# Kernel tuning notes

Hardware: AMD Instinct MI355X
Metric: run time of the kernel (lower is better)

Reference implementation:

```python
import jax, jax.numpy as jnp
import numpy as np

N_NODES = 100000
N_EDGES = 1600000
N_GRAPH = 100
IN_DIM = 64
LATENT = 128
STEPS = 2
MLP_LAYERS = 2
OUT_GLOBALS = 1
EPS = 1e-5  # haiku LayerNorm default


def setup_inputs() -> dict:
    key = jax.random.key(0)
    ks = jax.random.split(key, 8)
    nodes = jax.random.normal(ks[0], (N_NODES, IN_DIM), jnp.float32)
    senders = jax.random.randint(ks[1], (N_EDGES,), 0, N_NODES, jnp.int32)
    receivers = jax.random.randint(ks[2], (N_EDGES,), 0, N_NODES, jnp.int32)
    # 100 graphs of 1000 nodes each: jnp.repeat(arange(n_graph), n_node)
    graph_ids = (jnp.arange(N_NODES) // (N_NODES // N_GRAPH)).astype(jnp.int32)
    embed_w = jax.random.normal(ks[3], (IN_DIM, LATENT), jnp.float32) / np.sqrt(IN_DIM).astype(np.float32)
    embed_b = jnp.zeros((LATENT,), jnp.float32)
    mlp_w = jax.random.normal(ks[4], (STEPS, MLP_LAYERS, LATENT, LATENT), jnp.float32) / np.sqrt(LATENT).astype(np.float32)
    mlp_b = jnp.zeros((STEPS, MLP_LAYERS, LATENT), jnp.float32)
    ln_scale = jnp.ones((STEPS, LATENT), jnp.float32)
    ln_offset = jnp.zeros((STEPS, LATENT), jnp.float32)
    dec_w = jax.random.normal(ks[5], (LATENT, OUT_GLOBALS), jnp.float32) / np.sqrt(LATENT).astype(np.float32)
    dec_b = jnp.zeros((OUT_GLOBALS,), jnp.float32)
    return dict(nodes=nodes, senders=senders, receivers=receivers, graph_ids=graph_ids,
                embed_w=embed_w, embed_b=embed_b, mlp_w=mlp_w, mlp_b=mlp_b,
                ln_scale=ln_scale, ln_offset=ln_offset, dec_w=dec_w, dec_b=dec_b)


def _layernorm(x, scale, offset):
    mu = jnp.mean(x, axis=-1, keepdims=True)
    var = jnp.var(x, axis=-1, keepdims=True)
    return (x - mu) * jax.lax.rsqrt(var + EPS) * scale + offset


def reference(nodes, senders, receivers, graph_ids, embed_w, embed_b,
              mlp_w, mlp_b, ln_scale, ln_offset, dec_w, dec_b):
    n = nodes.shape[0]
    # jraph.GraphConvolution(add_self_edges=True, symmetric_normalization=True)
    self_loop = jnp.arange(n, dtype=senders.dtype)
    conv_s = jnp.concatenate([senders, self_loop])
    conv_r = jnp.concatenate([receivers, self_loop])
    ones_e = jnp.ones(conv_s.shape[0], jnp.float32)
    inv_sqrt_sdeg = jax.lax.rsqrt(jnp.maximum(jax.ops.segment_sum(ones_e, conv_s, n), 1.0))
    inv_sqrt_rdeg = jax.lax.rsqrt(jnp.maximum(jax.ops.segment_sum(ones_e, conv_r, n), 1.0))

    # embedder: hk.Linear on nodes
    h = nodes @ embed_w + embed_b

    for s in range(STEPS):
        # update_node_fn: MLP (dropout_rate=0 -> identity dropout)
        x = h
        for l in range(MLP_LAYERS):
            x = jax.nn.relu(x @ mlp_w[s, l] + mlp_b[s, l])
        # symmetric-normalized segment_sum aggregation with self-edges
        x = x * inv_sqrt_sdeg[:, None]
        x = jax.ops.segment_sum(x[conv_s], conv_r, num_segments=n)  # [n, LATENT]
        x = x * inv_sqrt_rdeg[:, None]
        h = x + h  # skip connection (add_graphs_tuples)
        h = _layernorm(h, ln_scale[s], ln_offset[s])

    # segment_mean pooling over graphs
    counts = jnp.maximum(jax.ops.segment_sum(jnp.ones(n, jnp.float32), graph_ids, N_GRAPH), 1.0)
    pooled = jax.ops.segment_sum(h, graph_ids, num_segments=N_GRAPH) / counts[:, None]
    # decoder: hk.Linear on pooled globals
    return pooled @ dec_w + dec_b  # [N_GRAPH, OUT_GLOBALS]
```

## Files before the change

kernel.cpp:

```cpp
#include <hip/hip_runtime.h>
#include <hip/hip_bf16.h>


#define N_NODES 100000
#define N_EDGES 1600000
#define N_GRAPH 100
#define NPG     1000
#define LATENT  128

#define NPART   4
#define PSIZE   (N_NODES / NPART)
#define NSLICE  64
#define ESLICE  (N_EDGES / NSLICE)

#define SCAN_CHUNK 2048
#define SCAN_NB    ((N_NODES + SCAN_CHUNK - 1) / SCAN_CHUNK)

typedef __attribute__((ext_vector_type(8))) short short8;
typedef __attribute__((ext_vector_type(4))) float f32x4;

__device__ __forceinline__ unsigned short f2bf(float f) {
    union { float f; unsigned int u; } v; v.f = f;
    unsigned int r = v.u + 0x7fff + ((v.u >> 16) & 1);
    return (unsigned short)(r >> 16);
}
__device__ __forceinline__ float bf2f(unsigned short u) {
    union { unsigned int u; float f; } v; v.u = ((unsigned int)u) << 16;
    return v.f;
}

__global__ __launch_bounds__(1024) void k_hist2(const int* __restrict__ senders,
                                                const int* __restrict__ receivers,
                                                unsigned short* __restrict__ ps16,
                                                unsigned short* __restrict__ pr16) {
    __shared__ unsigned int cs[PSIZE / 2];
    __shared__ unsigned int cr[PSIZE / 2];
    int rg = blockIdx.x & (NPART - 1), sl = blockIdx.x >> 2;
    int lo = rg * PSIZE;
    for (int i = threadIdx.x; i < PSIZE / 2; i += 1024) { cs[i] = 0; cr[i] = 0; }
    __syncthreads();
    int e0 = sl * ESLICE;
    for (int e = e0 + threadIdx.x; e < e0 + ESLICE; e += 1024) {
        int s = senders[e] - lo;
        if ((unsigned)s < PSIZE) atomicAdd(&cs[s >> 1], 1u << ((s & 1) * 16));
        int r = receivers[e] - lo;
        if ((unsigned)r < PSIZE) atomicAdd(&cr[r >> 1], 1u << ((r & 1) * 16));
    }
    __syncthreads();
    size_t base = (size_t)(rg * NSLICE + sl) * PSIZE;
    for (int i = threadIdx.x; i < PSIZE; i += 1024) {
        ps16[base + i] = (unsigned short)((cs[i >> 1] >> ((i & 1) * 16)) & 0xffff);
        pr16[base + i] = (unsigned short)((cr[i >> 1] >> ((i & 1) * 16)) & 0xffff);
    }
}

__global__ __launch_bounds__(256) void k_scan_slices(const unsigned short* __restrict__ ps16,
                                                     unsigned short* __restrict__ pr16,
                                                     int* __restrict__ deg_r,
                                                     float* __restrict__ inv_s,
                                                     float* __restrict__ inv_r) {
    int n = blockIdx.x * 256 + threadIdx.x;
    if (n >= N_NODES) return;
    int rg = n / PSIZE, i = n - rg * PSIZE;
    size_t base = (size_t)rg * NSLICE * PSIZE + i;
    int run = 0, ss = 0;
#pragma unroll 4
    for (int sl = 0; sl < NSLICE; sl++) {
        size_t idx = base + (size_t)sl * PSIZE;
        int v = pr16[idx];
        pr16[idx] = (unsigned short)run;
        run += v;
        ss += ps16[idx];
    }
    deg_r[n] = run;
    inv_r[n] = rsqrtf((float)(run + 1));
    inv_s[n] = rsqrtf((float)(ss + 1));
}

__global__ __launch_bounds__(256) void k_scan_block(const int* __restrict__ deg,
                                                    int* __restrict__ blocksums, int n) {
    int b = blockIdx.x, t = threadIdx.x;
    int base = b * SCAN_CHUNK + t * 8;
    int s = 0;
#pragma unroll
    for (int j = 0; j < 8; j++) { int i = base + j; if (i < n) s += deg[i]; }
    __shared__ int wsum[4];
#pragma unroll
    for (int off = 32; off > 0; off >>= 1) s += __shfl_down(s, off, 64);
    if ((t & 63) == 0) wsum[t >> 6] = s;
    __syncthreads();
    if (t == 0) blocksums[b] = wsum[0] + wsum[1] + wsum[2] + wsum[3];
}

__global__ __launch_bounds__(256) void k_scan_apply(const int* __restrict__ deg,
                                                    const int* __restrict__ blocksums,
                                                    int* __restrict__ row_start, int n) {
    __shared__ int boff_s;
    int b = blockIdx.x, t = threadIdx.x;
    if (t < 64) {
        int v = (t < b && t < SCAN_NB) ? blocksums[t] : 0;
#pragma unroll
        for (int off = 32; off > 0; off >>= 1) v += __shfl_down(v, off, 64);
        if (t == 0) boff_s = v;
    }
    int base = b * SCAN_CHUNK + t * 8;
    int v[8]; int tsum = 0;
#pragma unroll
    for (int j = 0; j < 8; j++) { int i = base + j; v[j] = (i < n) ? deg[i] : 0; tsum += v[j]; }
    __shared__ int wtot[4];
    int inc = tsum;
#pragma unroll
    for (int off = 1; off < 64; off <<= 1) {
        int u = __shfl_up(inc, off, 64);
        if ((t & 63) >= off) inc += u;
    }
    if ((t & 63) == 63) wtot[t >> 6] = inc;
    __syncthreads();
    int wbase = 0;
    for (int w = 0; w < (t >> 6); w++) wbase += wtot[w];
    int running = boff_s + wbase + (inc - tsum);
#pragma unroll
    for (int j = 0; j < 8; j++) {
        int i = base + j;
        if (i < n) {
            row_start[i] = running;
            running += v[j];
            if (i == n - 1) row_start[n] = running;
        }
    }
}

__global__ __launch_bounds__(1024) void k_fill2(const int* __restrict__ senders,
                                                const int* __restrict__ receivers,
                                                const unsigned short* __restrict__ pr16,
                                                const int* __restrict__ row_start,
                                                int* __restrict__ edge_src) {
    __shared__ int bs[PSIZE];
    int rg = blockIdx.x & (NPART - 1), sl = blockIdx.x >> 2;
    int lo = rg * PSIZE;
    const unsigned short* base = pr16 + (size_t)(rg * NSLICE + sl) * PSIZE;
    for (int i = threadIdx.x; i < PSIZE; i += 1024)
        bs[i] = row_start[lo + i] + (int)base[i];
    __syncthreads();
    int e0 = sl * ESLICE;
    for (int e = e0 + threadIdx.x; e < e0 + ESLICE; e += 1024) {
        int r = receivers[e] - lo;
        if ((unsigned)r < PSIZE) {
            int pos = atomicAdd(&bs[r], 1);
            edge_src[pos] = senders[e];
        }
    }
}

__global__ void k_wprep(const float* __restrict__ embed_w, const float* __restrict__ mlp_w,
                        unsigned short* __restrict__ hi, unsigned short* __restrict__ lo) {
    int t = blockIdx.x * 256 + threadIdx.x;
    if (t >= 8192 + 4 * 16384) return;
    const float* src; int local;
    if (t < 8192) { src = embed_w; local = t; }
    else { int m = t - 8192; src = mlp_w + (size_t)(m >> 14) * 16384; local = m & 16383; }
    int j = local & 7, lane = (local >> 3) & 63, tn = (local >> 9) & 7, kc = local >> 12;
    int k = kc * 32 + ((lane >> 4) << 3) + j;
    int n = tn * 16 + (lane & 15);
    float wv = src[k * 128 + n];
    unsigned short h = f2bf(wv);
    float rem = wv - bf2f(h);
    hi[t] = h; lo[t] = f2bf(rem);
}

__global__ __launch_bounds__(256) void k_embed_mlp(
    const float* __restrict__ A,
    const unsigned short* __restrict__ wehi, const unsigned short* __restrict__ welo,
    const float* __restrict__ eb,
    const unsigned short* __restrict__ w0hi, const unsigned short* __restrict__ w0lo,
    const unsigned short* __restrict__ w1hi, const unsigned short* __restrict__ w1lo,
    const float* __restrict__ b0, const float* __restrict__ b1,
    const float* __restrict__ inv_s,
    unsigned short* __restrict__ h16, unsigned short* __restrict__ x16, int M)
{
    __shared__ __align__(16) unsigned short t0[4][32][136];
    int t = threadIdx.x, w = t >> 6, L = t & 63;
    int m0 = blockIdx.x * 128 + w * 32;
    int lr = L & 15, lk = (L >> 4) * 8, lq = (L >> 4) * 4;

    float ebv[8], b0v[8], b1v[8];
#pragma unroll
    for (int tn = 0; tn < 8; tn++) {
        ebv[tn] = eb[tn * 16 + lr];
        b0v[tn] = b0[tn * 16 + lr];
        b1v[tn] = b1[tn * 16 + lr];
    }

    f32x4 acc[2][8];
#pragma unroll
    for (int bd = 0; bd < 2; bd++)
#pragma unroll
        for (int tn = 0; tn < 8; tn++) acc[bd][tn] = (f32x4){0.f, 0.f, 0.f, 0.f};
#pragma unroll
    for (int kc = 0; kc < 2; kc++) {
        short8 a[2];
#pragma unroll
        for (int bd = 0; bd < 2; bd++) {
            int grow = m0 + bd * 16 + lr; if (grow >= M) grow = M - 1;
            const float* rp = A + (size_t)grow * 64 + kc * 32 + lk;
            float4 v0 = *(const float4*)rp;
            float4 v1 = *(const float4*)(rp + 4);
            short8 pk;
            pk[0] = (short)f2bf(v0.x); pk[1] = (short)f2bf(v0.y);
            pk[2] = (short)f2bf(v0.z); pk[3] = (short)f2bf(v0.w);
            pk[4] = (short)f2bf(v1.x); pk[5] = (short)f2bf(v1.y);
            pk[6] = (short)f2bf(v1.z); pk[7] = (short)f2bf(v1.w);
            a[bd] = pk;
        }
#pragma unroll
        for (int tn = 0; tn < 8; tn++) {
            size_t fo = (size_t)(((kc * 8 + tn) * 64 + L)) * 8;
            short8 bh = *(const short8*)(wehi + fo);
            short8 bl = *(const short8*)(welo + fo);
#pragma unroll
            for (int bd = 0; bd < 2; bd++) {
                acc[bd][tn] = __builtin_amdgcn_mfma_f32_16x16x32_bf16(a[bd], bh, acc[bd][tn], 0, 0, 0);
                acc[bd][tn] = __builtin_amdgcn_mfma_f32_16x16x32_bf16(a[bd], bl, acc[bd][tn], 0, 0, 0);
            }
        }
    }
#pragma unroll
    for (int bd = 0; bd < 2; bd++)
#pragma unroll
        for (int tn = 0; tn < 8; tn++)
#pragma unroll
            for (int r = 0; r < 4; r++)
                t0[w][bd * 16 + lq + r][tn * 16 + lr] = f2bf(acc[bd][tn][r] + ebv[tn]);
#pragma unroll
    for (int q = 0; q < 8; q++) {
        int s = q * 64 + L;
        int row = s >> 4, c0 = (s & 15) * 8;
        int grow = m0 + row;
        if (grow < M)
            *(short8*)(h16 + (size_t)grow * 128 + c0) = *(const short8*)&t0[w][row][c0];
    }

#pragma unroll
    for (int bd = 0; bd < 2; bd++)
#pragma unroll
        for (int tn = 0; tn < 8; tn++) acc[bd][tn] = (f32x4){0.f, 0.f, 0.f, 0.f};
#pragma unroll
    for (int kc = 0; kc < 4; kc++) {
        short8 a[2];
#pragma unroll
        for (int bd = 0; bd < 2; bd++)
            a[bd] = *(const short8*)&t0[w][bd * 16 + lr][kc * 32 + lk];
#pragma unroll
        for (int tn = 0; tn < 8; tn++) {
            size_t fo = (size_t)(((kc * 8 + tn) * 64 + L)) * 8;
            short8 bh = *(const short8*)(w0hi + fo);
            short8 bl = *(const short8*)(w0lo + fo);
#pragma unroll
            for (int bd = 0; bd < 2; bd++) {
                acc[bd][tn] = __builtin_amdgcn_mfma_f32_16x16x32_bf16(a[bd], bh, acc[bd][tn], 0, 0, 0);
                acc[bd][tn] = __builtin_amdgcn_mfma_f32_16x16x32_bf16(a[bd], bl, acc[bd][tn], 0, 0, 0);
            }
        }
    }
#pragma unroll
    for (int bd = 0; bd < 2; bd++)
#pragma unroll
        for (int tn = 0; tn < 8; tn++)
#pragma unroll
            for (int r = 0; r < 4; r++)
                t0[w][bd * 16 + lq + r][tn * 16 + lr] = f2bf(fmaxf(acc[bd][tn][r] + b0v[tn], 0.f));

#pragma unroll
    for (int bd = 0; bd < 2; bd++)
#pragma unroll
        for (int tn = 0; tn < 8; tn++) acc[bd][tn] = (f32x4){0.f, 0.f, 0.f, 0.f};
#pragma unroll
    for (int kc = 0; kc < 4; kc++) {
        short8 a[2];
#pragma unroll
        for (int bd = 0; bd < 2; bd++)
            a[bd] = *(const short8*)&t0[w][bd * 16 + lr][kc * 32 + lk];
#pragma unroll
        for (int tn = 0; tn < 8; tn++) {
            size_t fo = (size_t)(((kc * 8 + tn) * 64 + L)) * 8;
            short8 bh = *(const short8*)(w1hi + fo);
            short8 bl = *(const short8*)(w1lo + fo);
#pragma unroll
            for (int bd = 0; bd < 2; bd++) {
                acc[bd][tn] = __builtin_amdgcn_mfma_f32_16x16x32_bf16(a[bd], bh, acc[bd][tn], 0, 0, 0);
                acc[bd][tn] = __builtin_amdgcn_mfma_f32_16x16x32_bf16(a[bd], bl, acc[bd][tn], 0, 0, 0);
            }
        }
    }
    float invs[2][4];
#pragma unroll
    for (int bd = 0; bd < 2; bd++)
#pragma unroll
        for (int r = 0; r < 4; r++) {
            int grow = m0 + bd * 16 + lq + r; if (grow >= M) grow = M - 1;
            invs[bd][r] = inv_s[grow];
        }
#pragma unroll
    for (int bd = 0; bd < 2; bd++)
#pragma unroll
        for (int tn = 0; tn < 8; tn++)
#pragma unroll
            for (int r = 0; r < 4; r++)
                t0[w][bd * 16 + lq + r][tn * 16 + lr] =
                    f2bf(fmaxf(acc[bd][tn][r] + b1v[tn], 0.f) * invs[bd][r]);
#pragma unroll
    for (int q = 0; q < 8; q++) {
        int s = q * 64 + L;
        int row = s >> 4, c0 = (s & 15) * 8;
        int grow = m0 + row;
        if (grow < M)
            *(short8*)(x16 + (size_t)grow * 128 + c0) = *(const short8*)&t0[w][row][c0];
    }
}

__global__ __launch_bounds__(256) void k_mlp(
    const unsigned short* __restrict__ A16, const unsigned short* __restrict__ w0hi,
    const unsigned short* __restrict__ w0lo, const unsigned short* __restrict__ w1hi,
    const unsigned short* __restrict__ w1lo, const float* __restrict__ b0,
    const float* __restrict__ b1, const float* __restrict__ inv_s,
    unsigned short* __restrict__ x16, int M)
{
    __shared__ __align__(16) unsigned short t1[4][32][136];
    int t = threadIdx.x, w = t >> 6, L = t & 63;
    int m0 = blockIdx.x * 128 + w * 32;
    int lr = L & 15, lk = (L >> 4) * 8, lq = (L >> 4) * 4;

    float b0v[8], b1v[8];
#pragma unroll
    for (int tn = 0; tn < 8; tn++) { b0v[tn] = b0[tn * 16 + lr]; b1v[tn] = b1[tn * 16 + lr]; }

    f32x4 acc[2][8];
#pragma unroll
    for (int bd = 0; bd < 2; bd++)
#pragma unroll
        for (int tn = 0; tn < 8; tn++) acc[bd][tn] = (f32x4){0.f, 0.f, 0.f, 0.f};

#pragma unroll
    for (int kc = 0; kc < 4; kc++) {
        short8 a[2];
#pragma unroll
        for (int bd = 0; bd < 2; bd++) {
            int grow = m0 + bd * 16 + lr; if (grow >= M) grow = M - 1;
            a[bd] = *(const short8*)(A16 + (size_t)grow * 128 + kc * 32 + lk);
        }
#pragma unroll
        for (int tn = 0; tn < 8; tn++) {
            size_t fo = (size_t)(((kc * 8 + tn) * 64 + L)) * 8;
            short8 bh = *(const short8*)(w0hi + fo);
            short8 bl = *(const short8*)(w0lo + fo);
#pragma unroll
            for (int bd = 0; bd < 2; bd++) {
                acc[bd][tn] = __builtin_amdgcn_mfma_f32_16x16x32_bf16(a[bd], bh, acc[bd][tn], 0, 0, 0);
                acc[bd][tn] = __builtin_amdgcn_mfma_f32_16x16x32_bf16(a[bd], bl, acc[bd][tn], 0, 0, 0);
            }
        }
    }
#pragma unroll
    for (int bd = 0; bd < 2; bd++)
#pragma unroll
        for (int tn = 0; tn < 8; tn++)
#pragma unroll
            for (int r = 0; r < 4; r++)
                t1[w][bd * 16 + lq + r][tn * 16 + lr] = f2bf(fmaxf(acc[bd][tn][r] + b0v[tn], 0.f));

    f32x4 acc2[2][8];
#pragma unroll
    for (int bd = 0; bd < 2; bd++)
#pragma unroll
        for (int tn = 0; tn < 8; tn++) acc2[bd][tn] = (f32x4){0.f, 0.f, 0.f, 0.f};
#pragma unroll
    for (int kc = 0; kc < 4; kc++) {
        short8 a[2];
#pragma unroll
        for (int bd = 0; bd < 2; bd++)
            a[bd] = *(const short8*)&t1[w][bd * 16 + lr][kc * 32 + lk];
#pragma unroll
        for (int tn = 0; tn < 8; tn++) {
            size_t fo = (size_t)(((kc * 8 + tn) * 64 + L)) * 8;
            short8 bh = *(const short8*)(w1hi + fo);
            short8 bl = *(const short8*)(w1lo + fo);
#pragma unroll
            for (int bd = 0; bd < 2; bd++) {
                acc2[bd][tn] = __builtin_amdgcn_mfma_f32_16x16x32_bf16(a[bd], bh, acc2[bd][tn], 0, 0, 0);
                acc2[bd][tn] = __builtin_amdgcn_mfma_f32_16x16x32_bf16(a[bd], bl, acc2[bd][tn], 0, 0, 0);
            }
        }
    }
    float invs[2][4];
#pragma unroll
    for (int bd = 0; bd < 2; bd++)
#pragma unroll
        for (int r = 0; r < 4; r++) {
            int grow = m0 + bd * 16 + lq + r; if (grow >= M) grow = M - 1;
            invs[bd][r] = inv_s[grow];
        }
#pragma unroll
    for (int bd = 0; bd < 2; bd++)
#pragma unroll
        for (int tn = 0; tn < 8; tn++)
#pragma unroll
            for (int r = 0; r < 4; r++)
                t1[w][bd * 16 + lq + r][tn * 16 + lr] =
                    f2bf(fmaxf(acc2[bd][tn][r] + b1v[tn], 0.f) * invs[bd][r]);
#pragma unroll
    for (int q = 0; q < 8; q++) {
        int s = q * 64 + L;
        int row = s >> 4, c0 = (s & 15) * 8;
        int grow = m0 + row;
        if (grow < M)
            *(short8*)(x16 + (size_t)grow * 128 + c0) = *(const short8*)&t1[w][row][c0];
    }
}

__global__ __launch_bounds__(256) void k_agg_ln(
    const unsigned short* __restrict__ x16, const int* __restrict__ row_start,
    const int* __restrict__ edge_src, const float* __restrict__ inv_r,
    const float* __restrict__ ln_scale, const float* __restrict__ ln_offset,
    unsigned short* __restrict__ h16)
{
    int node = __builtin_amdgcn_readfirstlane(blockIdx.x * 4 + (threadIdx.x >> 6));
    int L = threadIdx.x & 63;
    const unsigned int* x32 = (const unsigned int*)x16;
    const unsigned int* h32 = (const unsigned int*)h16;

    unsigned int su = x32[(size_t)node * 64 + L];
    float2 acc;
    acc.x = __uint_as_float(su << 16);
    acc.y = __uint_as_float(su & 0xffff0000u);

    int beg = row_start[node], end = row_start[node + 1];
    int j = beg;
    for (; j + 16 <= end; j += 16) {
        unsigned int u[16];
#pragma unroll
        for (int q = 0; q < 16; q++) u[q] = x32[(size_t)edge_src[j + q] * 64 + L];
#pragma unroll
        for (int q = 0; q < 16; q++) {
            acc.x += __uint_as_float(u[q] << 16);
            acc.y += __uint_as_float(u[q] & 0xffff0000u);
        }
    }
    for (; j + 8 <= end; j += 8) {
        unsigned int u[8];
#pragma unroll
        for (int q = 0; q < 8; q++) u[q] = x32[(size_t)edge_src[j + q] * 64 + L];
#pragma unroll
        for (int q = 0; q < 8; q++) {
            acc.x += __uint_as_float(u[q] << 16);
            acc.y += __uint_as_float(u[q] & 0xffff0000u);
        }
    }
    for (; j < end; j++) {
        unsigned int u0 = x32[(size_t)edge_src[j] * 64 + L];
        acc.x += __uint_as_float(u0 << 16);
        acc.y += __uint_as_float(u0 & 0xffff0000u);
    }

    float ir = inv_r[node];
    unsigned int hu = h32[(size_t)node * 64 + L];
    float y0 = acc.x * ir + __uint_as_float(hu << 16);
    float y1 = acc.y * ir + __uint_as_float(hu & 0xffff0000u);

    float s1 = y0 + y1, s2 = y0 * y0 + y1 * y1;
#pragma unroll
    for (int off = 32; off > 0; off >>= 1) {
        s1 += __shfl_xor(s1, off, 64);
        s2 += __shfl_xor(s2, off, 64);
    }
    float mu = s1 * (1.f / 128.f);
    float var = fmaxf(s2 * (1.f / 128.f) - mu * mu, 0.f);
    float rstd = rsqrtf(var + 1e-5f);
    float2 sc = *(const float2*)&ln_scale[L * 2];
    float2 of = *(const float2*)&ln_offset[L * 2];
    float ox = (y0 - mu) * rstd * sc.x + of.x;
    float oy = (y1 - mu) * rstd * sc.y + of.y;
    ((unsigned int*)h16)[(size_t)node * 64 + L] =
        (unsigned int)f2bf(ox) | ((unsigned int)f2bf(oy) << 16);
}

__global__ __launch_bounds__(256) void k_agg_pool(
    const unsigned short* __restrict__ x16, const int* __restrict__ row_start,
    const int* __restrict__ edge_src, const float* __restrict__ inv_r,
    const float* __restrict__ ln_scale, const float* __restrict__ ln_offset,
    const unsigned short* __restrict__ h16, float* __restrict__ poolpart)
{
    __shared__ float2 part[4][64];
    int w = threadIdx.x >> 6, L = threadIdx.x & 63;
    int node = __builtin_amdgcn_readfirstlane(blockIdx.x * 4 + w);
    const unsigned int* x32 = (const unsigned int*)x16;
    const unsigned int* h32 = (const unsigned int*)h16;

    unsigned int su = x32[(size_t)node * 64 + L];
    float2 acc;
    acc.x = __uint_as_float(su << 16);
    acc.y = __uint_as_float(su & 0xffff0000u);

    int beg = row_start[node], end = row_start[node + 1];
    int j = beg;
    for (; j + 16 <= end; j += 16) {
        unsigned int u[16];
#pragma unroll
        for (int q = 0; q < 16; q++) u[q] = x32[(size_t)edge_src[j + q] * 64 + L];
#pragma unroll
        for (int q = 0; q < 16; q++) {
            acc.x += __uint_as_float(u[q] << 16);
            acc.y += __uint_as_float(u[q] & 0xffff0000u);
        }
    }
    for (; j + 8 <= end; j += 8) {
        unsigned int u[8];
#pragma unroll
        for (int q = 0; q < 8; q++) u[q] = x32[(size_t)edge_src[j + q] * 64 + L];
#pragma unroll
        for (int q = 0; q < 8; q++) {
            acc.x += __uint_as_float(u[q] << 16);
            acc.y += __uint_as_float(u[q] & 0xffff0000u);
        }
    }
    for (; j < end; j++) {
        unsigned int u0 = x32[(size_t)edge_src[j] * 64 + L];
        acc.x += __uint_as_float(u0 << 16);
        acc.y += __uint_as_float(u0 & 0xffff0000u);
    }

    float ir = inv_r[node];
    unsigned int hu = h32[(size_t)node * 64 + L];
    float y0 = acc.x * ir + __uint_as_float(hu << 16);
    float y1 = acc.y * ir + __uint_as_float(hu & 0xffff0000u);

    float s1 = y0 + y1, s2 = y0 * y0 + y1 * y1;
#pragma unroll
    for (int off = 32; off > 0; off >>= 1) {
        s1 += __shfl_xor(s1, off, 64);
        s2 += __shfl_xor(s2, off, 64);
    }
    float mu = s1 * (1.f / 128.f);
    float var = fmaxf(s2 * (1.f / 128.f) - mu * mu, 0.f);
    float rstd = rsqrtf(var + 1e-5f);
    float2 sc = *(const float2*)&ln_scale[L * 2];
    float2 of = *(const float2*)&ln_offset[L * 2];
    float2 o;
    o.x = (y0 - mu) * rstd * sc.x + of.x;
    o.y = (y1 - mu) * rstd * sc.y + of.y;
    part[w][L] = o;
    __syncthreads();
    if (w == 0) {
        float2 p0 = part[0][L], p1 = part[1][L], p2 = part[2][L], p3 = part[3][L];
        float2 s;
        s.x = (p0.x + p1.x) + (p2.x + p3.x);
        s.y = (p0.y + p1.y) + (p2.y + p3.y);
        *(float2*)&poolpart[(size_t)blockIdx.x * 128 + L * 2] = s;
    }
}

__global__ __launch_bounds__(128) void k_pool2(const float* __restrict__ poolpart,
                                               float* __restrict__ poolpart2) {
    int b = blockIdx.x, col = threadIdx.x;
    const float* pg = poolpart + ((size_t)b * 25) * 128;
    float s = 0.f;
#pragma unroll
    for (int k = 0; k < 25; k++) s += pg[k * 128 + col];
    poolpart2[(size_t)b * 128 + col] = s;
}

__global__ __launch_bounds__(128) void k_pool3(const float* __restrict__ poolpart2,
                                               const float* __restrict__ dec_w,
                                               const float* __restrict__ dec_b,
                                               float* __restrict__ out) {
    int g = blockIdx.x, col = threadIdx.x;
    const float* pg = poolpart2 + (size_t)g * 10 * 128;
    float s = 0.f;
#pragma unroll
    for (int c = 0; c < 10; c++) s += pg[c * 128 + col];
    s = s * (1.f / (float)NPG) * dec_w[col];
    __shared__ float ws[2];
#pragma unroll
    for (int off = 32; off > 0; off >>= 1) s += __shfl_down(s, off, 64);
    if ((col & 63) == 0) ws[col >> 6] = s;
    __syncthreads();
    if (col == 0) out[g] = ws[0] + ws[1] + dec_b[0];
}

extern "C" void kernel_launch(void* const* d_in, const int* in_sizes, int n_in,
                              void* d_out, int out_size, void* d_ws, size_t ws_size,
                              hipStream_t stream) {
    (void)in_sizes; (void)n_in; (void)out_size; (void)ws_size;
    const float* nodes     = (const float*)d_in[0];
    const int*   senders   = (const int*)d_in[1];
    const int*   receivers = (const int*)d_in[2];
    const float* embed_w   = (const float*)d_in[4];
    const float* embed_b   = (const float*)d_in[5];
    const float* mlp_w     = (const float*)d_in[6];
    const float* mlp_b     = (const float*)d_in[7];
    const float* ln_scale  = (const float*)d_in[8];
    const float* ln_offset = (const float*)d_in[9];
    const float* dec_w     = (const float*)d_in[10];
    const float* dec_b     = (const float*)d_in[11];
    float* out = (float*)d_out;

    const int N = N_NODES;
    const int WF_TOTAL = 8192 + 4 * 16384;
    const size_t PART_TOTAL = (size_t)NPART * NSLICE * PSIZE;

    char* p = (char*)d_ws;
    auto alloc = [&](size_t bytes) -> void* {
        void* r = (void*)p;
        p += (bytes + 255) & ~(size_t)255;
        return r;
    };
    unsigned short* h16      = (unsigned short*)alloc((size_t)N * 128 * 2);
    unsigned short* x16      = (unsigned short*)alloc((size_t)N * 128 * 2);
    int*            edge_src = (int*)alloc((size_t)N_EDGES * 4);
    unsigned short* ps16     = (unsigned short*)alloc(PART_TOTAL * 2);
    unsigned short* pr16     = (unsigned short*)alloc(PART_TOTAL * 2);
    int*            deg_r    = (int*)alloc((size_t)N * 4);
    float*          inv_s    = (float*)alloc((size_t)N * 4);
    float*          inv_r    = (float*)alloc((size_t)N * 4);
    int*            row_start= (int*)alloc((size_t)(N + 1) * 4);
    int*            blocksums= (int*)alloc((size_t)SCAN_NB * 4);
    unsigned short* wfhi     = (unsigned short*)alloc((size_t)WF_TOTAL * 2);
    unsigned short* wflo     = (unsigned short*)alloc((size_t)WF_TOTAL * 2);
    float*          poolpart = (float*)alloc((size_t)(N / 4) * 128 * 4);
    float*          poolpart2= (float*)alloc((size_t)1000 * 128 * 4);

    k_wprep<<<(WF_TOTAL + 255) / 256, 256, 0, stream>>>(embed_w, mlp_w, wfhi, wflo);

    k_hist2<<<NPART * NSLICE, 1024, 0, stream>>>(senders, receivers, ps16, pr16);
    k_scan_slices<<<(N + 255) / 256, 256, 0, stream>>>(ps16, pr16, deg_r, inv_s, inv_r);
    k_scan_block<<<SCAN_NB, 256, 0, stream>>>(deg_r, blocksums, N);
    k_scan_apply<<<SCAN_NB, 256, 0, stream>>>(deg_r, blocksums, row_start, N);
    k_fill2<<<NPART * NSLICE, 1024, 0, stream>>>(senders, receivers, pr16, row_start, edge_src);

    int mblocks = (N + 127) / 128;
    const unsigned short* wehi = wfhi, *welo = wflo;
    const unsigned short* w0hi[2] = { wfhi + 8192,             wfhi + 8192 + 2 * 16384 };
    const unsigned short* w0lo[2] = { wflo + 8192,             wflo + 8192 + 2 * 16384 };
    const unsigned short* w1hi[2] = { wfhi + 8192 + 16384,     wfhi + 8192 + 3 * 16384 };
    const unsigned short* w1lo[2] = { wflo + 8192 + 16384,     wflo + 8192 + 3 * 16384 };

    k_embed_mlp<<<mblocks, 256, 0, stream>>>(nodes, wehi, welo, embed_b,
                                             w0hi[0], w0lo[0], w1hi[0], w1lo[0],
                                             mlp_b, mlp_b + 128, inv_s, h16, x16, N);
    k_agg_ln<<<N / 4, 256, 0, stream>>>(x16, row_start, edge_src, inv_r,
                                        ln_scale, ln_offset, h16);
    k_mlp<<<mblocks, 256, 0, stream>>>(h16, w0hi[1], w0lo[1], w1hi[1], w1lo[1],
                                       mlp_b + 256, mlp_b + 384, inv_s, x16, N);
    k_agg_pool<<<N / 4, 256, 0, stream>>>(x16, row_start, edge_src, inv_r,
                                          ln_scale + 128, ln_offset + 128, h16, poolpart);

    k_pool2<<<1000, 128, 0, stream>>>(poolpart, poolpart2);
    k_pool3<<<N_GRAPH, 128, 0, stream>>>(poolpart2, dec_w, dec_b, out);
}
```

Before: 392.7 us.

## Gather four neighbor rows per wave with 16-byte loads in aggregation

Restructures the neighbor gather in both aggregation kernels so each wave loads four source rows at once, with 16 lanes per row each doing a 16-byte load. Previously every lane issued a 4-byte load per edge. Partial sums are then combined across the lane groups with shuffles and redistributed through shared memory. This cuts the number of memory instructions and the load latency per edge, at the cost of more accumulator registers, the shuffle reduction, and an LDS round trip.

```diff
diff --git a/kernel.cpp b/kernel.cpp
--- a/kernel.cpp
+++ b/kernel.cpp
@@ -417,49 +417,93 @@
     }
 }
 
+__device__ __forceinline__ float2 agg_gather(const unsigned short* __restrict__ x16,
+                                             const int* __restrict__ edge_src,
+                                             int node, int L, int beg, int end,
+                                             float* redist)
+{
+    const unsigned int* x32 = (const unsigned int*)x16;
+    unsigned int su = x32[(size_t)node * 64 + L];
+    float2 accB;
+    accB.x = __uint_as_float(su << 16);
+    accB.y = __uint_as_float(su & 0xffff0000u);
+
+    float accA[8];
+#pragma unroll
+    for (int q = 0; q < 8; q++) accA[q] = 0.f;
+
+    int g = L >> 4;
+    int sub = (L & 15) * 16;
+    int j = beg;
+    for (; j + 16 <= end; j += 16) {
+        uint4 v[4];
+#pragma unroll
+        for (int b = 0; b < 4; b++) {
+            int i0 = edge_src[j + 4 * b + 0];
+            int i1 = edge_src[j + 4 * b + 1];
+            int i2 = edge_src[j + 4 * b + 2];
+            int i3 = edge_src[j + 4 * b + 3];
+            int src = (g == 0) ? i0 : (g == 1) ? i1 : (g == 2) ? i2 : i3;
+            v[b] = *(const uint4*)((const char*)x16 + (size_t)src * 256 + sub);
+        }
+#pragma unroll
+        for (int b = 0; b < 4; b++) {
+            accA[0] += __uint_as_float(v[b].x << 16);
+            accA[1] += __uint_as_float(v[b].x & 0xffff0000u);
+            accA[2] += __uint_as_float(v[b].y << 16);
+            accA[3] += __uint_as_float(v[b].y & 0xffff0000u);
+            accA[4] += __uint_as_float(v[b].z << 16);
+            accA[5] += __uint_as_float(v[b].z & 0xffff0000u);
+            accA[6] += __uint_as_float(v[b].w << 16);
+            accA[7] += __uint_as_float(v[b].w & 0xffff0000u);
+        }
+    }
+    for (; j + 4 <= end; j += 4) {
+        int i0 = edge_src[j], i1 = edge_src[j + 1], i2 = edge_src[j + 2], i3 = edge_src[j + 3];
+        int src = (g == 0) ? i0 : (g == 1) ? i1 : (g == 2) ? i2 : i3;
+        uint4 v = *(const uint4*)((const char*)x16 + (size_t)src * 256 + sub);
+        accA[0] += __uint_as_float(v.x << 16);
+        accA[1] += __uint_as_float(v.x & 0xffff0000u);
+        accA[2] += __uint_as_float(v.y << 16);
+        accA[3] += __uint_as_float(v.y & 0xffff0000u);
+        accA[4] += __uint_as_float(v.z << 16);
+        accA[5] += __uint_as_float(v.z & 0xffff0000u);
+        accA[6] += __uint_as_float(v.w << 16);
+        accA[7] += __uint_as_float(v.w & 0xffff0000u);
+    }
+    for (; j < end; j++) {
+        unsigned int u0 = x32[(size_t)edge_src[j] * 64 + L];
+        accB.x += __uint_as_float(u0 << 16);
+        accB.y += __uint_as_float(u0 & 0xffff0000u);
+    }
+#pragma unroll
+    for (int q = 0; q < 8; q++) {
+        accA[q] += __shfl_xor(accA[q], 16, 64);
+        accA[q] += __shfl_xor(accA[q], 32, 64);
+    }
+    if (L < 16) {
+#pragma unroll
+        for (int q = 0; q < 8; q++) redist[L * 8 + q] = accA[q];
+    }
+    float2 r;
+    r.x = accB.x + redist[L * 2];
+    r.y = accB.y + redist[L * 2 + 1];
+    return r;
+}
+
 __global__ __launch_bounds__(256) void k_agg_ln(
     const unsigned short* __restrict__ x16, const int* __restrict__ row_start,
     const int* __restrict__ edge_src, const float* __restrict__ inv_r,
     const float* __restrict__ ln_scale, const float* __restrict__ ln_offset,
     unsigned short* __restrict__ h16)
 {
-    int node = __builtin_amdgcn_readfirstlane(blockIdx.x * 4 + (threadIdx.x >> 6));
-    int L = threadIdx.x & 63;
-    const unsigned int* x32 = (const unsigned int*)x16;
+    __shared__ float redist[4][128];
+    int w = threadIdx.x >> 6, L = threadIdx.x & 63;
+    int node = __builtin_amdgcn_readfirstlane(blockIdx.x * 4 + w);
     const unsigned int* h32 = (const unsigned int*)h16;
 
-    unsigned int su = x32[(size_t)node * 64 + L];
-    float2 acc;
-    acc.x = __uint_as_float(su << 16);
-    acc.y = __uint_as_float(su & 0xffff0000u);
-
     int beg = row_start[node], end = row_start[node + 1];
-    int j = beg;
-    for (; j + 16 <= end; j += 16) {
-        unsigned int u[16];
-#pragma unroll
-        for (int q = 0; q < 16; q++) u[q] = x32[(size_t)edge_src[j + q] * 64 + L];
-#pragma unroll
-        for (int q = 0; q < 16; q++) {
-            acc.x += __uint_as_float(u[q] << 16);
-            acc.y += __uint_as_float(u[q] & 0xffff0000u);
-        }
-    }
-    for (; j + 8 <= end; j += 8) {
-        unsigned int u[8];
-#pragma unroll
-        for (int q = 0; q < 8; q++) u[q] = x32[(size_t)edge_src[j + q] * 64 + L];
-#pragma unroll
-        for (int q = 0; q < 8; q++) {
-            acc.x += __uint_as_float(u[q] << 16);
-            acc.y += __uint_as_float(u[q] & 0xffff0000u);
-        }
-    }
-    for (; j < end; j++) {
-        unsigned int u0 = x32[(size_t)edge_src[j] * 64 + L];
-        acc.x += __uint_as_float(u0 << 16);
-        acc.y += __uint_as_float(u0 & 0xffff0000u);
-    }
+    float2 acc = agg_gather(x16, edge_src, node, L, beg, end, redist[w]);
 
     float ir = inv_r[node];
     unsigned int hu = h32[(size_t)node * 64 + L];
@@ -489,44 +533,14 @@
     const float* __restrict__ ln_scale, const float* __restrict__ ln_offset,
     const unsigned short* __restrict__ h16, float* __restrict__ poolpart)
 {
+    __shared__ float redist[4][128];
     __shared__ float2 part[4][64];
     int w = threadIdx.x >> 6, L = threadIdx.x & 63;
     int node = __builtin_amdgcn_readfirstlane(blockIdx.x * 4 + w);
-    const unsigned int* x32 = (const unsigned int*)x16;
     const unsigned int* h32 = (const unsigned int*)h16;
 
-    unsigned int su = x32[(size_t)node * 64 + L];
-    float2 acc;
-    acc.x = __uint_as_float(su << 16);
-    acc.y = __uint_as_float(su & 0xffff0000u);
-
     int beg = row_start[node], end = row_start[node + 1];
-    int j = beg;
-    for (; j + 16 <= end; j += 16) {
-        unsigned int u[16];
-#pragma unroll
-        for (int q = 0; q < 16; q++) u[q] = x32[(size_t)edge_src[j + q] * 64 + L];
-#pragma unroll
-        for (int q = 0; q < 16; q++) {
-            acc.x += __uint_as_float(u[q] << 16);
-            acc.y += __uint_as_float(u[q] & 0xffff0000u);
-        }
-    }
-    for (; j + 8 <= end; j += 8) {
-        unsigned int u[8];
-#pragma unroll
-        for (int q = 0; q < 8; q++) u[q] = x32[(size_t)edge_src[j + q] * 64 + L];
-#pragma unroll
-        for (int q = 0; q < 8; q++) {
-            acc.x += __uint_as_float(u[q] << 16);
-            acc.y += __uint_as_float(u[q] & 0xffff0000u);
-        }
-    }
-    for (; j < end; j++) {
-        unsigned int u0 = x32[(size_t)edge_src[j] * 64 + L];
-        acc.x += __uint_as_float(u0 << 16);
-        acc.y += __uint_as_float(u0 & 0xffff0000u);
-    }
+    float2 acc = agg_gather(x16, edge_src, node, L, beg, end, redist[w]);
 
     float ir = inv_r[node];
     unsigned int hu = h32[(size_t)node * 64 + L];
```

Result: no change. 393.8 us (+0.3%).
